# Optimization experiments

Measured on AMD Instinct MI355X. Metric: run time of the kernel, lower is better.

## Reference

```python
import jax, jax.numpy as jnp
import numpy as np


def _gcn_norm(edge_index, num_nodes, dtype):
    # Add self-loops and compute symmetric normalization deg^-1/2 * deg^-1/2
    loop = jnp.arange(num_nodes, dtype=edge_index.dtype)
    src = jnp.concatenate([edge_index[0], loop])
    dst = jnp.concatenate([edge_index[1], loop])
    ew = jnp.ones(src.shape[0], dtype=dtype)
    deg = jax.ops.segment_sum(ew, dst, num_segments=num_nodes)
    dinv = jnp.where(deg > 0, jax.lax.rsqrt(deg), 0.0).astype(dtype)
    norm = dinv[src] * dinv[dst]  # [E+N]
    return src, dst, norm


def _gcn_layer(h, src, dst, norm, W, b, num_nodes):
    h = h @ W                              # [N, out] dense transform
    msg = h[src] * norm[:, None]           # gather + scale  [E+N, out]
    out = jax.ops.segment_sum(msg, dst, num_segments=num_nodes)  # scatter-add
    return jax.nn.relu(out + b)            # bias + activation (ReLU)


def setup_inputs() -> dict:
    key = jax.random.key(0)
    ks = jax.random.split(key, 8)
    N, E, D, H = 100000, 640000, 128, 256
    x = jax.random.normal(ks[0], (N, D), dtype=jnp.float32)
    edge_index = jax.random.randint(ks[1], (2, E), 0, N, dtype=jnp.int64)
    W0 = jax.random.normal(ks[2], (D, H), dtype=jnp.float32) * (1.0 / np.sqrt(D))
    b0 = jnp.zeros((H,), dtype=jnp.float32)
    W1 = jax.random.normal(ks[3], (H, H), dtype=jnp.float32) * (1.0 / np.sqrt(H))
    b1 = jnp.zeros((H,), dtype=jnp.float32)
    W2 = jax.random.normal(ks[4], (H, H), dtype=jnp.float32) * (1.0 / np.sqrt(H))
    b2 = jnp.zeros((H,), dtype=jnp.float32)
    return {"x": x, "edge_index": edge_index, "W0": W0, "b0": b0,
            "W1": W1, "b1": b1, "W2": W2, "b2": b2}


def reference(x, edge_index, W0, b0, W1, b1, W2, b2):
    N = x.shape[0]
    src, dst, norm = _gcn_norm(edge_index, N, x.dtype)
    z = _gcn_layer(x, src, dst, norm, W0, b0, N)
    z = _gcn_layer(z, src, dst, norm, W1, b1, N)
    z = _gcn_layer(z, src, dst, norm, W2, b2, N)
    return z
```

## Files before the change

### kernel.cpp

```cpp
#include <hip/hip_runtime.h>
#include <hip/hip_fp16.h>


typedef __bf16 bf16x8 __attribute__((ext_vector_type(8)));
typedef float  f32x4  __attribute__((ext_vector_type(4)));
typedef unsigned short ushort_t;
typedef unsigned int   uint_t;

__device__ __forceinline__ ushort_t f2bf(float f) {
    uint_t u = __builtin_bit_cast(uint_t, f);
    u += 0x7FFFu + ((u >> 16) & 1u);
    return (ushort_t)(u >> 16);
}
__device__ __forceinline__ float bf2f(ushort_t h) {
    uint_t u = ((uint_t)h) << 16;
    return __builtin_bit_cast(float, u);
}
__device__ __forceinline__ float4 h4_to_f4(uint2 u) {
    __half2 a = __builtin_bit_cast(__half2, u.x);
    __half2 b = __builtin_bit_cast(__half2, u.y);
    float2 fa = __half22float2(a);
    float2 fb = __half22float2(b);
    return make_float4(fa.x, fa.y, fb.x, fb.y);
}

__global__ void k_detect(const int* __restrict__ ei, int E, int* __restrict__ flag) {
    __shared__ int nonzero;
    if (threadIdx.x == 0) nonzero = 0;
    __syncthreads();
    size_t k = (size_t)threadIdx.x * (size_t)E / 256;
    if (ei[2 * k + 1] != 0) atomicOr(&nonzero, 1);
    __syncthreads();
    if (threadIdx.x == 0) *flag = (nonzero == 0) ? 1 : 0;
}

__global__ __launch_bounds__(256) void k_convert(const int* __restrict__ ei, int E,
                                                 const int* __restrict__ flag,
                                                 int* __restrict__ src32,
                                                 int* __restrict__ dst32) {
    int is64 = *flag;
    for (int e = blockIdx.x * 256 + threadIdx.x; e < E; e += gridDim.x * 256) {
        if (is64) {
            const long long* p = (const long long*)ei;
            src32[e] = (int)p[e];
            dst32[e] = (int)p[(size_t)E + e];
        } else {
            src32[e] = ei[e];
            dst32[e] = ei[(size_t)E + e];
        }
    }
}

__global__ __launch_bounds__(256) void k_zero_int(int* __restrict__ p, int n) {
    for (int i = blockIdx.x * 256 + threadIdx.x; i < n; i += gridDim.x * 256) p[i] = 0;
}

__global__ __launch_bounds__(256) void k_count(const int* __restrict__ dst,
                                               int* __restrict__ indeg, int E) {
    for (int e = blockIdx.x * 256 + threadIdx.x; e < E; e += gridDim.x * 256)
        atomicAdd(&indeg[dst[e]], 1);
}

__global__ __launch_bounds__(256) void k_dinv(const int* __restrict__ indeg,
                                              float* __restrict__ dinv, int N) {
    int i = blockIdx.x * 256 + threadIdx.x;
    if (i < N) dinv[i] = rsqrtf(1.0f + (float)indeg[i]);
}

__global__ __launch_bounds__(256) void k_scan1(const int* __restrict__ indeg,
                                               int* __restrict__ rowptr,
                                               int* __restrict__ partials, int N) {
    __shared__ int sdata[256];
    const int b = blockIdx.x, t = threadIdx.x;
    const int base = b * 1024 + t * 4;
    int v[4], s = 0;
#pragma unroll
    for (int j = 0; j < 4; ++j) { v[j] = (base + j < N) ? indeg[base + j] : 0; s += v[j]; }
    sdata[t] = s;
    __syncthreads();
    for (int off = 1; off < 256; off <<= 1) {
        int x = (t >= off) ? sdata[t - off] : 0;
        __syncthreads();
        sdata[t] += x;
        __syncthreads();
    }
    int run = (t > 0) ? sdata[t - 1] : 0;
    if (t == 255) partials[b] = sdata[255];
#pragma unroll
    for (int j = 0; j < 4; ++j) {
        if (base + j < N) rowptr[base + j] = run;
        run += v[j];
    }
}

__global__ __launch_bounds__(256) void k_scan2(int* __restrict__ partials, int nb) {
    __shared__ int sdata[256];
    int t = threadIdx.x;
    sdata[t] = (t < nb) ? partials[t] : 0;
    __syncthreads();
    for (int off = 1; off < 256; off <<= 1) {
        int x = (t >= off) ? sdata[t - off] : 0;
        __syncthreads();
        sdata[t] += x;
        __syncthreads();
    }
    if (t < nb) partials[t] = (t > 0) ? sdata[t - 1] : 0;
}

__global__ __launch_bounds__(256) void k_scan3(int* __restrict__ rowptr,
                                               const int* __restrict__ partials,
                                               int N, int E) {
    for (int i = blockIdx.x * 256 + threadIdx.x; i < N; i += gridDim.x * 256)
        rowptr[i] += partials[i >> 10];
    if (blockIdx.x == 0 && threadIdx.x == 0) rowptr[N] = E;
}

__global__ __launch_bounds__(256) void k_fill(const int* __restrict__ src,
                                              const int* __restrict__ dst,
                                              const int* __restrict__ rowptr,
                                              const float* __restrict__ dinv,
                                              int* __restrict__ fillcnt,
                                              int* __restrict__ colsrc,
                                              float* __restrict__ colnorm, int E) {
    for (int e = blockIdx.x * 256 + threadIdx.x; e < E; e += gridDim.x * 256) {
        int d = dst[e], s = src[e];
        int pos = rowptr[d] + atomicAdd(&fillcnt[d], 1);
        colsrc[pos]  = s;
        colnorm[pos] = dinv[s] * dinv[d];
    }
}

__global__ __launch_bounds__(256) void k_wsplit(const float* __restrict__ W,
                                                ushort_t* __restrict__ Wh,
                                                ushort_t* __restrict__ Wl,
                                                int K, int Nn) {
    int idx = blockIdx.x * 256 + threadIdx.x;
    if (idx >= K * Nn) return;
    int k = idx / Nn, n = idx - k * Nn;
    float w = W[idx];
    ushort_t h = f2bf(w);
    ushort_t l = f2bf(w - bf2f(h));
    Wh[(size_t)n * K + k] = h;
    Wl[(size_t)n * K + k] = l;
}

__global__ __launch_bounds__(256) void k_agg_f32(const float* __restrict__ z,
                                                 const int* __restrict__ rowptr,
                                                 const int* __restrict__ colsrc,
                                                 const float* __restrict__ colnorm,
                                                 const float* __restrict__ dinv,
                                                 ushort_t* __restrict__ oh,
                                                 ushort_t* __restrict__ ol, int N) {
    constexpr int C = 128;
    const int node = (int)(((size_t)blockIdx.x * 256 + threadIdx.x) >> 6);
    const int lane = threadIdx.x & 63;
    if (node >= N) return;
    const float di = dinv[node];
    float a0[2], a1[2];
    {
        const float s2 = di * di;
        float2 zv = *(const float2*)&z[(size_t)node * C + lane * 2];
        a0[0] = zv.x * s2; a0[1] = zv.y * s2; a1[0] = a1[1] = 0.f;
    }
    const int start = rowptr[node], end = rowptr[node + 1];
    for (int base = start; base < end; base += 64) {
        const int rem = end - base;
        int sv = 0; float nv = 0.f;
        if (lane < rem) { sv = colsrc[base + lane]; nv = colnorm[base + lane]; }
        const int cnt = rem < 64 ? rem : 64;
        int jj = 0;
        for (; jj + 2 <= cnt; jj += 2) {
            int   s0 = __shfl(sv, jj),  s1 = __shfl(sv, jj + 1);
            float n0 = __shfl(nv, jj),  n1 = __shfl(nv, jj + 1);
            float2 v0 = *(const float2*)&z[(size_t)s0 * C + lane * 2];
            float2 v1 = *(const float2*)&z[(size_t)s1 * C + lane * 2];
            a0[0] = fmaf(v0.x, n0, a0[0]); a0[1] = fmaf(v0.y, n0, a0[1]);
            a1[0] = fmaf(v1.x, n1, a1[0]); a1[1] = fmaf(v1.y, n1, a1[1]);
        }
        if (jj < cnt) {
            int   s0 = __shfl(sv, jj);
            float n0 = __shfl(nv, jj);
            float2 v0 = *(const float2*)&z[(size_t)s0 * C + lane * 2];
            a0[0] = fmaf(v0.x, n0, a0[0]); a0[1] = fmaf(v0.y, n0, a0[1]);
        }
    }
    ushort_t h[2], l[2];
#pragma unroll
    for (int j = 0; j < 2; ++j) {
        float a = a0[j] + a1[j];
        h[j] = f2bf(a);
        l[j] = f2bf(a - bf2f(h[j]));
    }
    size_t ob = (size_t)node * C + lane * 2;
    *(uint_t*)&oh[ob] = (uint_t)h[0] | ((uint_t)h[1] << 16);
    *(uint_t*)&ol[ob] = (uint_t)l[0] | ((uint_t)l[1] << 16);
}

__global__ __launch_bounds__(256) void k_agg_f16(const __half* __restrict__ z,
                                                 const int* __restrict__ rowptr,
                                                 const int* __restrict__ colsrc,
                                                 const float* __restrict__ colnorm,
                                                 const float* __restrict__ dinv,
                                                 ushort_t* __restrict__ oh,
                                                 ushort_t* __restrict__ ol, int N) {
    constexpr int C = 256;
    const int node = (int)(((size_t)blockIdx.x * 256 + threadIdx.x) >> 6);
    const int lane = threadIdx.x & 63;
    if (node >= N) return;
    const float di = dinv[node];
    float a0[4], a1[4];
    {
        const float s2 = di * di;
        float4 zv = h4_to_f4(*(const uint2*)&z[(size_t)node * C + lane * 4]);
        a0[0] = zv.x * s2; a0[1] = zv.y * s2; a0[2] = zv.z * s2; a0[3] = zv.w * s2;
        a1[0] = a1[1] = a1[2] = a1[3] = 0.f;
    }
    const int start = rowptr[node], end = rowptr[node + 1];
    for (int base = start; base < end; base += 64) {
        const int rem = end - base;
        int sv = 0; float nv = 0.f;
        if (lane < rem) { sv = colsrc[base + lane]; nv = colnorm[base + lane]; }
        const int cnt = rem < 64 ? rem : 64;
        int jj = 0;
        for (; jj + 2 <= cnt; jj += 2) {
            int   s0 = __shfl(sv, jj),  s1 = __shfl(sv, jj + 1);
            float n0 = __shfl(nv, jj),  n1 = __shfl(nv, jj + 1);
            uint2 u0 = *(const uint2*)&z[(size_t)s0 * C + lane * 4];
            uint2 u1 = *(const uint2*)&z[(size_t)s1 * C + lane * 4];
            float4 v0 = h4_to_f4(u0);
            float4 v1 = h4_to_f4(u1);
            a0[0] = fmaf(v0.x, n0, a0[0]); a0[1] = fmaf(v0.y, n0, a0[1]);
            a0[2] = fmaf(v0.z, n0, a0[2]); a0[3] = fmaf(v0.w, n0, a0[3]);
            a1[0] = fmaf(v1.x, n1, a1[0]); a1[1] = fmaf(v1.y, n1, a1[1]);
            a1[2] = fmaf(v1.z, n1, a1[2]); a1[3] = fmaf(v1.w, n1, a1[3]);
        }
        if (jj < cnt) {
            int   s0 = __shfl(sv, jj);
            float n0 = __shfl(nv, jj);
            float4 v0 = h4_to_f4(*(const uint2*)&z[(size_t)s0 * C + lane * 4]);
            a0[0] = fmaf(v0.x, n0, a0[0]); a0[1] = fmaf(v0.y, n0, a0[1]);
            a0[2] = fmaf(v0.z, n0, a0[2]); a0[3] = fmaf(v0.w, n0, a0[3]);
        }
    }
    ushort_t h[4], l[4];
#pragma unroll
    for (int j = 0; j < 4; ++j) {
        float a = a0[j] + a1[j];
        h[j] = f2bf(a);
        l[j] = f2bf(a - bf2f(h[j]));
    }
    size_t ob = (size_t)node * C + lane * 4;
    uint2 hv, lv;
    hv.x = (uint_t)h[0] | ((uint_t)h[1] << 16);
    hv.y = (uint_t)h[2] | ((uint_t)h[3] << 16);
    lv.x = (uint_t)l[0] | ((uint_t)l[1] << 16);
    lv.y = (uint_t)l[2] | ((uint_t)l[3] << 16);
    *(uint2*)&oh[ob] = hv;
    *(uint2*)&ol[ob] = lv;
}

template <typename OutT>
__global__ __launch_bounds__(256, 2) void k_gemm_mfma(
    const ushort_t* __restrict__ Ah, const ushort_t* __restrict__ Al,
    const ushort_t* __restrict__ Bh, const ushort_t* __restrict__ Bl,
    const float* __restrict__ bias, OutT* __restrict__ C,
    int M, int K, int Nn) {
    __shared__ ushort_t As[2][128][72];
    __shared__ ushort_t Bs[2][128][72];
    const int tid  = threadIdx.x;
    const int lane = tid & 63;
    const int wid  = tid >> 6;
    const int wr   = wid >> 1, wc = wid & 1;
    const int bm   = blockIdx.x * 128;
    const int bn   = blockIdx.y * 128;
    const int srow = tid >> 3;
    const int sk8  = tid & 7;

    f32x4 acc[4][4] = {};

    for (int kt = 0; kt < K; kt += 64) {
        __syncthreads();
#pragma unroll
        for (int j = 0; j < 4; ++j) {
            int row = srow + j * 32;
            uint4 vh = make_uint4(0, 0, 0, 0), vl = vh;
            int gr = bm + row;
            if (gr < M) {
                vh = *(const uint4*)&Ah[(size_t)gr * K + kt + sk8 * 8];
                vl = *(const uint4*)&Al[(size_t)gr * K + kt + sk8 * 8];
            }
            *(uint4*)&As[0][row][sk8 * 8] = vh;
            *(uint4*)&As[1][row][sk8 * 8] = vl;
            uint4 wh = *(const uint4*)&Bh[(size_t)(bn + row) * K + kt + sk8 * 8];
            uint4 wl = *(const uint4*)&Bl[(size_t)(bn + row) * K + kt + sk8 * 8];
            *(uint4*)&Bs[0][row][sk8 * 8] = wh;
            *(uint4*)&Bs[1][row][sk8 * 8] = wl;
        }
        __syncthreads();
#pragma unroll
        for (int ks = 0; ks < 2; ++ks) {
            const int acol = ks * 32 + ((lane >> 4) << 3);
            const int ar   = (wr << 6) + (lane & 15);
            const int br   = (wc << 6) + (lane & 15);
            bf16x8 ah[4], al[4], bh[4], bl[4];
#pragma unroll
            for (int t4 = 0; t4 < 4; ++t4) {
                ah[t4] = *(const bf16x8*)&As[0][ar + t4 * 16][acol];
                al[t4] = *(const bf16x8*)&As[1][ar + t4 * 16][acol];
                bh[t4] = *(const bf16x8*)&Bs[0][br + t4 * 16][acol];
                bl[t4] = *(const bf16x8*)&Bs[1][br + t4 * 16][acol];
            }
#pragma unroll
            for (int mt = 0; mt < 4; ++mt)
#pragma unroll
                for (int nt = 0; nt < 4; ++nt) {
                    acc[mt][nt] = __builtin_amdgcn_mfma_f32_16x16x32_bf16(
                        ah[mt], bh[nt], acc[mt][nt], 0, 0, 0);
                    acc[mt][nt] = __builtin_amdgcn_mfma_f32_16x16x32_bf16(
                        ah[mt], bl[nt], acc[mt][nt], 0, 0, 0);
                    acc[mt][nt] = __builtin_amdgcn_mfma_f32_16x16x32_bf16(
                        al[mt], bh[nt], acc[mt][nt], 0, 0, 0);
                }
        }
    }

    const int col0  = bn + (wc << 6) + (lane & 15);
    const int rbase = bm + (wr << 6) + ((lane >> 4) << 2);
    float bv[4];
#pragma unroll
    for (int nt = 0; nt < 4; ++nt) bv[nt] = bias[col0 + nt * 16];
#pragma unroll
    for (int mt = 0; mt < 4; ++mt)
#pragma unroll
        for (int j = 0; j < 4; ++j) {
            int r = rbase + mt * 16 + j;
            if (r < M) {
                OutT* cp = &C[(size_t)r * Nn + col0];
#pragma unroll
                for (int nt = 0; nt < 4; ++nt) {
                    float v = fmaxf(acc[mt][nt][j] + bv[nt], 0.f);
                    if constexpr (sizeof(OutT) == 2)
                        cp[nt * 16] = __float2half_rn(v);
                    else
                        cp[nt * 16] = v;
                }
            }
        }
}

extern "C" void kernel_launch(void* const* d_in, const int* in_sizes, int n_in,
                              void* d_out, int out_size, void* d_ws, size_t ws_size,
                              hipStream_t stream) {
    const float* x  = (const float*)d_in[0];
    const int*   ei = (const int*)d_in[1];
    const float* W0 = (const float*)d_in[2];
    const float* b0 = (const float*)d_in[3];
    const float* W1 = (const float*)d_in[4];
    const float* b1 = (const float*)d_in[5];
    const float* W2 = (const float*)d_in[6];
    const float* b2 = (const float*)d_in[7];

    const int D = 128, H = 256;
    const int N = in_sizes[0] / D;
    const int E = in_sizes[1] / 2;

    char* ws = (char*)d_ws;
    auto align = [](size_t v) { return (v + 511) & ~(size_t)511; };
    size_t o = 0;
    int*      flag     = (int*)(ws + o);      o += align(sizeof(int));
    float*    dinv     = (float*)(ws + o);    o += align((size_t)N * 4);
    int*      indeg    = (int*)(ws + o);      o += align((size_t)N * 4);
    int*      fillcnt  = (int*)(ws + o);      o += align((size_t)N * 4);
    int*      rowptr   = (int*)(ws + o);      o += align(((size_t)N + 1) * 4);
    int*      partials = (int*)(ws + o);      o += align(256 * 4);
    int*      src32    = (int*)(ws + o);      o += align((size_t)E * 4);
    int*      dst32    = (int*)(ws + o);      o += align((size_t)E * 4);
    int*      colsrc   = (int*)(ws + o);      o += align((size_t)E * 4);
    float*    colnorm  = (float*)(ws + o);    o += align((size_t)E * 4);
    ushort_t* Wth      = (ushort_t*)(ws + o); o += align((size_t)H * H * 2);
    ushort_t* Wtl      = (ushort_t*)(ws + o); o += align((size_t)H * H * 2);
    ushort_t* Wth2     = (ushort_t*)(ws + o); o += align((size_t)H * H * 2);
    ushort_t* Wtl2     = (ushort_t*)(ws + o); o += align((size_t)H * H * 2);
    ushort_t* Wth3     = (ushort_t*)(ws + o); o += align((size_t)H * H * 2);
    ushort_t* Wtl3     = (ushort_t*)(ws + o); o += align((size_t)H * H * 2);
    ushort_t* Ah       = (ushort_t*)(ws + o); o += align((size_t)N * H * 2);
    ushort_t* Al       = (ushort_t*)(ws + o); o += align((size_t)N * H * 2);
    __half*   z16      = (__half*)(ws + o);   o += align((size_t)N * H * 2);
    float*    out      = (float*)d_out;

    const int nBlkN  = (N + 255) / 256;
    const int nBlkE  = (E + 255) / 256;
    const int nbScan = (N + 1023) / 1024;

    k_detect<<<1, 256, 0, stream>>>(ei, E, flag);
    k_convert<<<nBlkE, 256, 0, stream>>>(ei, E, flag, src32, dst32);
    k_zero_int<<<nBlkN, 256, 0, stream>>>(indeg, N);
    k_zero_int<<<nBlkN, 256, 0, stream>>>(fillcnt, N);
    k_count<<<nBlkE, 256, 0, stream>>>(dst32, indeg, E);
    k_dinv<<<nBlkN, 256, 0, stream>>>(indeg, dinv, N);
    k_scan1<<<nbScan, 256, 0, stream>>>(indeg, rowptr, partials, N);
    k_scan2<<<1, 256, 0, stream>>>(partials, nbScan);
    k_scan3<<<nBlkN, 256, 0, stream>>>(rowptr, partials, N, E);
    k_fill<<<nBlkE, 256, 0, stream>>>(src32, dst32, rowptr, dinv, fillcnt,
                                      colsrc, colnorm, E);

    k_wsplit<<<(D * H + 255) / 256, 256, 0, stream>>>(W0, Wth, Wtl, D, H);
    k_wsplit<<<(H * H + 255) / 256, 256, 0, stream>>>(W1, Wth2, Wtl2, H, H);
    k_wsplit<<<(H * H + 255) / 256, 256, 0, stream>>>(W2, Wth3, Wtl3, H, H);

    const int aggBlk = (N * 64 + 255) / 256;
    dim3 gemmGrid((N + 127) / 128, H / 128);

    k_agg_f32<<<aggBlk, 256, 0, stream>>>(x, rowptr, colsrc, colnorm,
                                          dinv, Ah, Al, N);
    k_gemm_mfma<__half><<<gemmGrid, 256, 0, stream>>>(Ah, Al, Wth, Wtl, b0,
                                                      z16, N, D, H);

    k_agg_f16<<<aggBlk, 256, 0, stream>>>(z16, rowptr, colsrc, colnorm,
                                          dinv, Ah, Al, N);
    k_gemm_mfma<__half><<<gemmGrid, 256, 0, stream>>>(Ah, Al, Wth2, Wtl2, b1,
                                                      z16, N, H, H);

    k_agg_f16<<<aggBlk, 256, 0, stream>>>(z16, rowptr, colsrc, colnorm,
                                          dinv, Ah, Al, N);
    k_gemm_mfma<float><<<gemmGrid, 256, 0, stream>>>(Ah, Al, Wth3, Wtl3, b2,
                                                     out, N, H, H);

    (void)n_in; (void)out_size; (void)ws_size; (void)o;
}
```

Baseline: 585.1 us.

## Convert input features to fp16 before aggregation and read GEMM weights directly from global

Adds a pass that converts x to fp16 so the first aggregation gathers half-width rows, and merges the two aggregation kernels into one template. The GEMM no longer stages weight tiles in shared memory. Each wave now loads its B fragments straight from global memory (weights are small and cache-resident), which halves LDS use and raises launch_bounds occupancy to 4 blocks. The risks are an extra conversion pass over x, reduced precision of x in the first layer, and more global/L2 traffic for the weight reads.

Result: slower. 735.8 us (+25.7%).

```diff
diff --git a/kernel.cpp b/kernel.cpp
--- a/kernel.cpp
+++ b/kernel.cpp
@@ -22,6 +22,10 @@
     float2 fa = __half22float2(a);
     float2 fb = __half22float2(b);
     return make_float4(fa.x, fa.y, fb.x, fb.y);
+}
+__device__ __forceinline__ float2 h2_to_f2(uint_t u) {
+    __half2 a = __builtin_bit_cast(__half2, u);
+    return __half22float2(a);
 }
 
 __global__ void k_detect(const int* __restrict__ ei, int E, int* __restrict__ flag) {
@@ -144,23 +148,45 @@
     Wl[(size_t)n * K + k] = l;
 }
 
-__global__ __launch_bounds__(256) void k_agg_f32(const float* __restrict__ z,
+__global__ __launch_bounds__(256) void k_x2h(const float* __restrict__ x,
+                                             __half* __restrict__ xh, size_t n4) {
+    for (size_t i = (size_t)blockIdx.x * 256 + threadIdx.x; i < n4;
+         i += (size_t)gridDim.x * 256) {
+        float4 v = *(const float4*)&x[i * 4];
+        __half2 a = __floats2half2_rn(v.x, v.y);
+        __half2 b = __floats2half2_rn(v.z, v.w);
+        uint2 u;
+        u.x = __builtin_bit_cast(uint_t, a);
+        u.y = __builtin_bit_cast(uint_t, b);
+        *(uint2*)&xh[i * 4] = u;
+    }
+}
+
+template <int C>
+__global__ __launch_bounds__(256) void k_agg_f16(const __half* __restrict__ z,
                                                  const int* __restrict__ rowptr,
                                                  const int* __restrict__ colsrc,
                                                  const float* __restrict__ colnorm,
                                                  const float* __restrict__ dinv,
                                                  ushort_t* __restrict__ oh,
                                                  ushort_t* __restrict__ ol, int N) {
-    constexpr int C = 128;
+    constexpr int VE = C / 64;
     const int node = (int)(((size_t)blockIdx.x * 256 + threadIdx.x) >> 6);
     const int lane = threadIdx.x & 63;
     if (node >= N) return;
     const float di = dinv[node];
-    float a0[2], a1[2];
+    float a0[VE], a1[VE];
     {
         const float s2 = di * di;
-        float2 zv = *(const float2*)&z[(size_t)node * C + lane * 2];
-        a0[0] = zv.x * s2; a0[1] = zv.y * s2; a1[0] = a1[1] = 0.f;
+        if constexpr (VE == 4) {
+            float4 zv = h4_to_f4(*(const uint2*)&z[(size_t)node * C + lane * 4]);
+            a0[0] = zv.x * s2; a0[1] = zv.y * s2; a0[2] = zv.z * s2; a0[3] = zv.w * s2;
+            a1[0] = a1[1] = a1[2] = a1[3] = 0.f;
+        } else {
+            float2 zv = h2_to_f2(*(const uint_t*)&z[(size_t)node * C + lane * 2]);
+            a0[0] = zv.x * s2; a0[1] = zv.y * s2;
+            a1[0] = a1[1] = 0.f;
+        }
     }
     const int start = rowptr[node], end = rowptr[node + 1];
     for (int base = start; base < end; base += 64) {
@@ -172,101 +198,62 @@
         for (; jj + 2 <= cnt; jj += 2) {
             int   s0 = __shfl(sv, jj),  s1 = __shfl(sv, jj + 1);
             float n0 = __shfl(nv, jj),  n1 = __shfl(nv, jj + 1);
-            float2 v0 = *(const float2*)&z[(size_t)s0 * C + lane * 2];
-            float2 v1 = *(const float2*)&z[(size_t)s1 * C + lane * 2];
-            a0[0] = fmaf(v0.x, n0, a0[0]); a0[1] = fmaf(v0.y, n0, a0[1]);
-            a1[0] = fmaf(v1.x, n1, a1[0]); a1[1] = fmaf(v1.y, n1, a1[1]);
+            if constexpr (VE == 4) {
+                float4 v0 = h4_to_f4(*(const uint2*)&z[(size_t)s0 * C + lane * 4]);
+                float4 v1 = h4_to_f4(*(const uint2*)&z[(size_t)s1 * C + lane * 4]);
+                a0[0] = fmaf(v0.x, n0, a0[0]); a0[1] = fmaf(v0.y, n0, a0[1]);
+                a0[2] = fmaf(v0.z, n0, a0[2]); a0[3] = fmaf(v0.w, n0, a0[3]);
+                a1[0] = fmaf(v1.x, n1, a1[0]); a1[1] = fmaf(v1.y, n1, a1[1]);
+                a1[2] = fmaf(v1.z, n1, a1[2]); a1[3] = fmaf(v1.w, n1, a1[3]);
+            } else {
+                float2 v0 = h2_to_f2(*(const uint_t*)&z[(size_t)s0 * C + lane * 2]);
+                float2 v1 = h2_to_f2(*(const uint_t*)&z[(size_t)s1 * C + lane * 2]);
+                a0[0] = fmaf(v0.x, n0, a0[0]); a0[1] = fmaf(v0.y, n0, a0[1]);
+                a1[0] = fmaf(v1.x, n1, a1[0]); a1[1] = fmaf(v1.y, n1, a1[1]);
+            }
         }
         if (jj < cnt) {
             int   s0 = __shfl(sv, jj);
             float n0 = __shfl(nv, jj);
-            float2 v0 = *(const float2*)&z[(size_t)s0 * C + lane * 2];
-            a0[0] = fmaf(v0.x, n0, a0[0]); a0[1] = fmaf(v0.y, n0, a0[1]);
-        }
-    }
-    ushort_t h[2], l[2];
-#pragma unroll
-    for (int j = 0; j < 2; ++j) {
+            if constexpr (VE == 4) {
+                float4 v0 = h4_to_f4(*(const uint2*)&z[(size_t)s0 * C + lane * 4]);
+                a0[0] = fmaf(v0.x, n0, a0[0]); a0[1] = fmaf(v0.y, n0, a0[1]);
+                a0[2] = fmaf(v0.z, n0, a0[2]); a0[3] = fmaf(v0.w, n0, a0[3]);
+            } else {
+                float2 v0 = h2_to_f2(*(const uint_t*)&z[(size_t)s0 * C + lane * 2]);
+                a0[0] = fmaf(v0.x, n0, a0[0]); a0[1] = fmaf(v0.y, n0, a0[1]);
+            }
+        }
+    }
+    ushort_t h[VE], l[VE];
+#pragma unroll
+    for (int j = 0; j < VE; ++j) {
         float a = a0[j] + a1[j];
         h[j] = f2bf(a);
         l[j] = f2bf(a - bf2f(h[j]));
     }
-    size_t ob = (size_t)node * C + lane * 2;
-    *(uint_t*)&oh[ob] = (uint_t)h[0] | ((uint_t)h[1] << 16);
-    *(uint_t*)&ol[ob] = (uint_t)l[0] | ((uint_t)l[1] << 16);
-}
-
-__global__ __launch_bounds__(256) void k_agg_f16(const __half* __restrict__ z,
-                                                 const int* __restrict__ rowptr,
-                                                 const int* __restrict__ colsrc,
-                                                 const float* __restrict__ colnorm,
-                                                 const float* __restrict__ dinv,
-                                                 ushort_t* __restrict__ oh,
-                                                 ushort_t* __restrict__ ol, int N) {
-    constexpr int C = 256;
-    const int node = (int)(((size_t)blockIdx.x * 256 + threadIdx.x) >> 6);
-    const int lane = threadIdx.x & 63;
-    if (node >= N) return;
-    const float di = dinv[node];
-    float a0[4], a1[4];
-    {
-        const float s2 = di * di;
-        float4 zv = h4_to_f4(*(const uint2*)&z[(size_t)node * C + lane * 4]);
-        a0[0] = zv.x * s2; a0[1] = zv.y * s2; a0[2] = zv.z * s2; a0[3] = zv.w * s2;
-        a1[0] = a1[1] = a1[2] = a1[3] = 0.f;
-    }
-    const int start = rowptr[node], end = rowptr[node + 1];
-    for (int base = start; base < end; base += 64) {
-        const int rem = end - base;
-        int sv = 0; float nv = 0.f;
-        if (lane < rem) { sv = colsrc[base + lane]; nv = colnorm[base + lane]; }
-        const int cnt = rem < 64 ? rem : 64;
-        int jj = 0;
-        for (; jj + 2 <= cnt; jj += 2) {
-            int   s0 = __shfl(sv, jj),  s1 = __shfl(sv, jj + 1);
-            float n0 = __shfl(nv, jj),  n1 = __shfl(nv, jj + 1);
-            uint2 u0 = *(const uint2*)&z[(size_t)s0 * C + lane * 4];
-            uint2 u1 = *(const uint2*)&z[(size_t)s1 * C + lane * 4];
-            float4 v0 = h4_to_f4(u0);
-            float4 v1 = h4_to_f4(u1);
-            a0[0] = fmaf(v0.x, n0, a0[0]); a0[1] = fmaf(v0.y, n0, a0[1]);
-            a0[2] = fmaf(v0.z, n0, a0[2]); a0[3] = fmaf(v0.w, n0, a0[3]);
-            a1[0] = fmaf(v1.x, n1, a1[0]); a1[1] = fmaf(v1.y, n1, a1[1]);
-            a1[2] = fmaf(v1.z, n1, a1[2]); a1[3] = fmaf(v1.w, n1, a1[3]);
-        }
-        if (jj < cnt) {
-            int   s0 = __shfl(sv, jj);
-            float n0 = __shfl(nv, jj);
-            float4 v0 = h4_to_f4(*(const uint2*)&z[(size_t)s0 * C + lane * 4]);
-            a0[0] = fmaf(v0.x, n0, a0[0]); a0[1] = fmaf(v0.y, n0, a0[1]);
-            a0[2] = fmaf(v0.z, n0, a0[2]); a0[3] = fmaf(v0.w, n0, a0[3]);
-        }
-    }
-    ushort_t h[4], l[4];
-#pragma unroll
-    for (int j = 0; j < 4; ++j) {
-        float a = a0[j] + a1[j];
-        h[j] = f2bf(a);
-        l[j] = f2bf(a - bf2f(h[j]));
-    }
-    size_t ob = (size_t)node * C + lane * 4;
-    uint2 hv, lv;
-    hv.x = (uint_t)h[0] | ((uint_t)h[1] << 16);
-    hv.y = (uint_t)h[2] | ((uint_t)h[3] << 16);
-    lv.x = (uint_t)l[0] | ((uint_t)l[1] << 16);
-    lv.y = (uint_t)l[2] | ((uint_t)l[3] << 16);
-    *(uint2*)&oh[ob] = hv;
-    *(uint2*)&ol[ob] = lv;
+    size_t ob = (size_t)node * C + lane * VE;
+    if constexpr (VE == 4) {
+        uint2 hv, lv;
+        hv.x = (uint_t)h[0] | ((uint_t)h[1] << 16);
+        hv.y = (uint_t)h[2] | ((uint_t)h[3] << 16);
+        lv.x = (uint_t)l[0] | ((uint_t)l[1] << 16);
+        lv.y = (uint_t)l[2] | ((uint_t)l[3] << 16);
+        *(uint2*)&oh[ob] = hv;
+        *(uint2*)&ol[ob] = lv;
+    } else {
+        *(uint_t*)&oh[ob] = (uint_t)h[0] | ((uint_t)h[1] << 16);
+        *(uint_t*)&ol[ob] = (uint_t)l[0] | ((uint_t)l[1] << 16);
+    }
 }
 
 template <typename OutT>
-__global__ __launch_bounds__(256, 2) void k_gemm_mfma(
+__global__ __launch_bounds__(256, 4) void k_gemm_mfma(
     const ushort_t* __restrict__ Ah, const ushort_t* __restrict__ Al,
     const ushort_t* __restrict__ Bh, const ushort_t* __restrict__ Bl,
     const float* __restrict__ bias, OutT* __restrict__ C,
     int M, int K, int Nn) {
     __shared__ ushort_t As[2][128][72];
-    __shared__ ushort_t Bs[2][128][72];
     const int tid  = threadIdx.x;
     const int lane = tid & 63;
     const int wid  = tid >> 6;
@@ -291,36 +278,33 @@
             }
             *(uint4*)&As[0][row][sk8 * 8] = vh;
             *(uint4*)&As[1][row][sk8 * 8] = vl;
-            uint4 wh = *(const uint4*)&Bh[(size_t)(bn + row) * K + kt + sk8 * 8];
-            uint4 wl = *(const uint4*)&Bl[(size_t)(bn + row) * K + kt + sk8 * 8];
-            *(uint4*)&Bs[0][row][sk8 * 8] = wh;
-            *(uint4*)&Bs[1][row][sk8 * 8] = wl;
         }
         __syncthreads();
 #pragma unroll
         for (int ks = 0; ks < 2; ++ks) {
             const int acol = ks * 32 + ((lane >> 4) << 3);
             const int ar   = (wr << 6) + (lane & 15);
-            const int br   = (wc << 6) + (lane & 15);
-            bf16x8 ah[4], al[4], bh[4], bl[4];
+            bf16x8 ah[4], al[4];
 #pragma unroll
             for (int t4 = 0; t4 < 4; ++t4) {
                 ah[t4] = *(const bf16x8*)&As[0][ar + t4 * 16][acol];
                 al[t4] = *(const bf16x8*)&As[1][ar + t4 * 16][acol];
-                bh[t4] = *(const bf16x8*)&Bs[0][br + t4 * 16][acol];
-                bl[t4] = *(const bf16x8*)&Bs[1][br + t4 * 16][acol];
-            }
-#pragma unroll
-            for (int mt = 0; mt < 4; ++mt)
-#pragma unroll
-                for (int nt = 0; nt < 4; ++nt) {
+            }
+#pragma unroll
+            for (int nt = 0; nt < 4; ++nt) {
+                const size_t gn = (size_t)(bn + (wc << 6) + nt * 16 + (lane & 15));
+                bf16x8 bh = *(const bf16x8*)&Bh[gn * K + kt + acol];
+                bf16x8 bl = *(const bf16x8*)&Bl[gn * K + kt + acol];
+#pragma unroll
+                for (int mt = 0; mt < 4; ++mt) {
                     acc[mt][nt] = __builtin_amdgcn_mfma_f32_16x16x32_bf16(
-                        ah[mt], bh[nt], acc[mt][nt], 0, 0, 0);
+                        ah[mt], bh, acc[mt][nt], 0, 0, 0);
                     acc[mt][nt] = __builtin_amdgcn_mfma_f32_16x16x32_bf16(
-                        ah[mt], bl[nt], acc[mt][nt], 0, 0, 0);
+                        ah[mt], bl, acc[mt][nt], 0, 0, 0);
                     acc[mt][nt] = __builtin_amdgcn_mfma_f32_16x16x32_bf16(
-                        al[mt], bh[nt], acc[mt][nt], 0, 0, 0);
+                        al[mt], bh, acc[mt][nt], 0, 0, 0);
                 }
+            }
         }
     }
 
@@ -386,6 +370,7 @@
     ushort_t* Ah       = (ushort_t*)(ws + o); o += align((size_t)N * H * 2);
     ushort_t* Al       = (ushort_t*)(ws + o); o += align((size_t)N * H * 2);
     __half*   z16      = (__half*)(ws + o);   o += align((size_t)N * H * 2);
+    __half*   x16      = (__half*)(ws + o);   o += align((size_t)N * D * 2);
     float*    out      = (float*)d_out;
 
     const int nBlkN  = (N + 255) / 256;
@@ -407,22 +392,23 @@
     k_wsplit<<<(D * H + 255) / 256, 256, 0, stream>>>(W0, Wth, Wtl, D, H);
     k_wsplit<<<(H * H + 255) / 256, 256, 0, stream>>>(W1, Wth2, Wtl2, H, H);
     k_wsplit<<<(H * H + 255) / 256, 256, 0, stream>>>(W2, Wth3, Wtl3, H, H);
+    k_x2h<<<2048, 256, 0, stream>>>(x, x16, (size_t)N * D / 4);
 
     const int aggBlk = (N * 64 + 255) / 256;
     dim3 gemmGrid((N + 127) / 128, H / 128);
 
-    k_agg_f32<<<aggBlk, 256, 0, stream>>>(x, rowptr, colsrc, colnorm,
-                                          dinv, Ah, Al, N);
+    k_agg_f16<128><<<aggBlk, 256, 0, stream>>>(x16, rowptr, colsrc, colnorm,
+                                               dinv, Ah, Al, N);
     k_gemm_mfma<__half><<<gemmGrid, 256, 0, stream>>>(Ah, Al, Wth, Wtl, b0,
                                                       z16, N, D, H);
 
-    k_agg_f16<<<aggBlk, 256, 0, stream>>>(z16, rowptr, colsrc, colnorm,
-                                          dinv, Ah, Al, N);
+    k_agg_f16<256><<<aggBlk, 256, 0, stream>>>(z16, rowptr, colsrc, colnorm,
+                                               dinv, Ah, Al, N);
     k_gemm_mfma<__half><<<gemmGrid, 256, 0, stream>>>(Ah, Al, Wth2, Wtl2, b1,
                                                       z16, N, H, H);
 
-    k_agg_f16<<<aggBlk, 256, 0, stream>>>(z16, rowptr, colsrc, colnorm,
-                                          dinv, Ah, Al, N);
+    k_agg_f16<256><<<aggBlk, 256, 0, stream>>>(z16, rowptr, colsrc, colnorm,
+                                               dinv, Ah, Al, N);
     k_gemm_mfma<float><<<gemmGrid, 256, 0, stream>>>(Ah, Al, Wth3, Wtl3, b2,
                                                      out, N, H, H);
 
```
